# Kernel optimization log

Measured on AMD Instinct MI355X. Metric: run time of the kernel, lower is better.

The kernel has to match this reference:

```python
import jax, jax.numpy as jnp
import numpy as np

N = 50000          # total nodes in batch
E = 800000         # total edges (avg degree 16)
G = 512            # number of graphs in batch
H = 64             # hidden_channels
L = 5              # num_layers
C_IN = 1           # in_channels
NUM_CLASSES = 2
BN_EPS = 1e-5


def setup_inputs() -> dict:
    key = jax.random.key(0)
    ks = jax.random.split(key, 12)
    x = jax.random.normal(ks[0], (N, C_IN), dtype=jnp.float32)
    edge_index = jax.random.randint(ks[1], (2, E), 0, N, dtype=jnp.int64)
    batch = jnp.sort(jax.random.randint(ks[2], (N,), 0, G, dtype=jnp.int64))
    s = 0.1
    # GINConv MLP params: layer0 input is C_IN, layers 1..4 input is H
    w1_0 = jax.random.normal(ks[3], (C_IN, H), dtype=jnp.float32) * s
    w1_rest = jax.random.normal(ks[4], (L - 1, H, H), dtype=jnp.float32) * s
    b1 = jax.random.normal(ks[5], (L, H), dtype=jnp.float32) * s
    gamma_mlp = jnp.ones((L, H), dtype=jnp.float32)
    beta_mlp = jnp.zeros((L, H), dtype=jnp.float32)
    w2 = jax.random.normal(ks[6], (L, H, H), dtype=jnp.float32) * s
    b2 = jax.random.normal(ks[7], (L, H), dtype=jnp.float32) * s
    # outer per-layer BatchNorm (BasicGNN norm) params
    gamma = jnp.ones((L, H), dtype=jnp.float32)
    beta = jnp.zeros((L, H), dtype=jnp.float32)
    lin_w = jax.random.normal(ks[8], (C_IN + H * L, NUM_CLASSES), dtype=jnp.float32) * s
    lin_b = jnp.zeros((NUM_CLASSES,), dtype=jnp.float32)
    return dict(x=x, edge_index=edge_index, batch=batch, w1_0=w1_0,
                w1_rest=w1_rest, b1=b1, gamma_mlp=gamma_mlp, beta_mlp=beta_mlp,
                w2=w2, b2=b2, gamma=gamma, beta=beta, lin_w=lin_w, lin_b=lin_b)


def _bn(h, g, b):
    # training-mode batch norm over the node axis (biased variance, as torch)
    mu = h.mean(axis=0)
    var = h.var(axis=0)
    return (h - mu) * jax.lax.rsqrt(var + BN_EPS) * g + b


def _gin_backbone(x, src, dst, w1_0, w1_rest, b1, gm, bm, w2, b2, go, bo):
    h = x
    outs = []
    for l in range(L):  # fixed small layer count
        agg = jax.ops.segment_sum(h[src], dst, num_segments=N)  # sum_{j->i} h_j
        z = h + agg  # (1+eps)*h_i + agg, eps=0
        w1 = w1_0 if l == 0 else w1_rest[l - 1]
        z = z @ w1 + b1[l]
        z = jax.nn.relu(_bn(z, gm[l], bm[l]))   # MLP inner norm+act
        z = z @ w2[l] + b2[l]
        z = jax.nn.relu(_bn(z, go[l], bo[l]))   # BasicGNN norm+act (jk set)
        h = z
        outs.append(h)
    return jnp.concatenate(outs, axis=1)  # jk='cat' -> [N, H*L]


def reference(x, edge_index, batch, w1_0, w1_rest, b1, gamma_mlp, beta_mlp,
              w2, b2, gamma, beta, lin_w, lin_b):
    src, dst = edge_index[0], edge_index[1]
    node_desc = _gin_backbone(x, src, dst, w1_0, w1_rest, b1,
                              gamma_mlp, beta_mlp, w2, b2, gamma, beta)
    graph_desc = jax.ops.segment_sum(node_desc, batch, num_segments=G)  # [G, H*L]
    first_desc = jax.ops.segment_sum(x, batch, num_segments=G)          # [G, C_IN]
    gdesc = jnp.concatenate((first_desc, graph_desc), axis=1)           # [G, C_IN+H*L]
    # final dropout is identity in eval mode
    return gdesc @ lin_w + lin_b
```

## Files before the change

### kernel.cpp

```cpp
#include <hip/hip_runtime.h>

#define NN 50000
#define NE 800000
#define NG 512
#define HC 64
#define NL 5
#define GD_COLS 321
#define BN_EPS 1e-5f
#define DEG_CAP 64

#define SLICE 6250
#define ECHUNK 3125

typedef unsigned short bf16_t;
typedef unsigned int uiv4 __attribute__((ext_vector_type(4)));
typedef __attribute__((ext_vector_type(8))) short short8v;
typedef __attribute__((ext_vector_type(4))) float f32x4;
typedef __attribute__((ext_vector_type(4))) unsigned uint4v;

static __device__ __forceinline__ unsigned f2bfbits(float f) {
    unsigned u = __float_as_uint(f);
    return (u + 0x7FFFu + ((u >> 16) & 1u)) >> 16;
}
static __device__ __forceinline__ bf16_t f2bf(float f) { return (bf16_t)f2bfbits(f); }
static __device__ __forceinline__ float bf2f(bf16_t h) {
    return __uint_as_float(((unsigned)h) << 16);
}
static __device__ __forceinline__ float bflo(unsigned w) { return __uint_as_float(w << 16); }
static __device__ __forceinline__ float bfhi(unsigned w) {
    return __uint_as_float(w & 0xffff0000u);
}

static __device__ __forceinline__ void mfma_gemm_phase(
    const unsigned* zw, const unsigned* wsm, const float* __restrict__ bias,
    bf16_t* __restrict__ out, float* __restrict__ statsOut, float (*redS)[64],
    float (*redQ)[64], int r0, int t, int lane, int wid) {
    int l15 = lane & 15, l4 = lane >> 4;
    int tr = wid >> 1;
    int tc0 = (wid & 1) * 2;
    f32x4 d0 = {0.f, 0.f, 0.f, 0.f}, d1 = {0.f, 0.f, 0.f, 0.f};
    const unsigned* arow = &zw[(tr * 16 + l15) * 33];
    const unsigned* brow0 = &wsm[(tc0 * 16 + l15) * 33];
    const unsigned* brow1 = &wsm[((tc0 + 1) * 16 + l15) * 33];
#pragma unroll
    for (int kc = 0; kc < 2; ++kc) {
        int kb = kc * 16 + l4 * 4;
        uint4v aw = {arow[kb], arow[kb + 1], arow[kb + 2], arow[kb + 3]};
        uint4v bw0 = {brow0[kb], brow0[kb + 1], brow0[kb + 2], brow0[kb + 3]};
        uint4v bw1 = {brow1[kb], brow1[kb + 1], brow1[kb + 2], brow1[kb + 3]};
        short8v af = __builtin_bit_cast(short8v, aw);
        d0 = __builtin_amdgcn_mfma_f32_16x16x32_bf16(af, __builtin_bit_cast(short8v, bw0), d0,
                                                     0, 0, 0);
        d1 = __builtin_amdgcn_mfma_f32_16x16x32_bf16(af, __builtin_bit_cast(short8v, bw1), d1,
                                                     0, 0, 0);
    }
    int c0 = tc0 * 16 + l15, c1 = c0 + 16;
    float bv0 = bias[c0], bv1 = bias[c1];
    float s0 = 0.f, q0 = 0.f, s1 = 0.f, q1 = 0.f;
#pragma unroll
    for (int j = 0; j < 4; ++j) {
        int gr = r0 + tr * 16 + l4 * 4 + j;
        if (gr < NN) {
            float v0 = d0[j] + bv0, v1 = d1[j] + bv1;
            out[(size_t)gr * HC + c0] = f2bf(v0);
            out[(size_t)gr * HC + c1] = f2bf(v1);
            s0 += v0;
            q0 += v0 * v0;
            s1 += v1;
            q1 += v1 * v1;
        }
    }
    s0 += __shfl_xor(s0, 16); s0 += __shfl_xor(s0, 32);
    q0 += __shfl_xor(q0, 16); q0 += __shfl_xor(q0, 32);
    s1 += __shfl_xor(s1, 16); s1 += __shfl_xor(s1, 32);
    q1 += __shfl_xor(q1, 16); q1 += __shfl_xor(q1, 32);
    if (l4 == 0) { redS[wid][c0] = s0; redQ[wid][c0] = q0; }
    else if (l4 == 1) { redS[wid][c1] = s1; redQ[wid][c1] = q1; }
    else if (l4 == 2) { redS[wid][c0 ^ 32] = 0.f; redQ[wid][c0 ^ 32] = 0.f; }
    else { redS[wid][c1 ^ 32] = 0.f; redQ[wid][c1 ^ 32] = 0.f; }
    __syncthreads();
    if (t < 64) {
        float ts = 0.f, t2 = 0.f;
#pragma unroll
        for (int k = 0; k < 8; ++k) {
            ts += redS[k][t];
            t2 += redQ[k][t];
        }
        atomicAdd(&statsOut[t], ts);
        atomicAdd(&statsOut[64 + t], t2);
    }
}

__global__ __launch_bounds__(256) void scatter_kernel(const int* __restrict__ ei,
                                                      int* __restrict__ cnt,
                                                      unsigned short* __restrict__ ssrc,
                                                      float* __restrict__ stats,
                                                      float* __restrict__ gdesc) {
    int t = threadIdx.x;
    int g = blockIdx.x & 7;
    int c = blockIdx.x >> 3;
    int gt = blockIdx.x * 256 + t;
    int total = gridDim.x * 256;
    for (int i = gt; i < NL * 256; i += total) stats[i] = 0.f;
    for (int i = gt; i < NG * GD_COLS; i += total) gdesc[i] = 0.f;
    int lo = g * SLICE, hi = lo + SLICE;
    int e0 = c * ECHUNK;
    int e1 = e0 + ECHUNK;
    if (e1 > NE) e1 = NE;
    for (int e = e0 + t; e < e1; e += 256) {
        int d = ei[NE + e];
        if (d >= lo && d < hi) {
            int s = ei[e];
            int pos = atomicAdd(&cnt[d], 1);
            if (pos < DEG_CAP) ssrc[(d << 6) + pos] = (unsigned short)s;
        }
    }
}

__global__ __launch_bounds__(256) void layer0_kernel(
    const float* __restrict__ x, const int* __restrict__ cnt,
    const unsigned short* __restrict__ ssrc, const float* __restrict__ w,
    const float* __restrict__ bias, const int* __restrict__ batch, float* __restrict__ gdesc,
    bf16_t* __restrict__ y, float* __restrict__ stats) {
    __shared__ float z0p[256];
    __shared__ float z0s[64];
    int t = threadIdx.x, lane = t & 63, wid = t >> 6;
    int r0 = blockIdx.x * 64;
    if (t < 64) {
        int i = r0 + t;
        if (i < NN) atomicAdd(&gdesc[batch[i] * GD_COLS], x[i]);
    }
    {
        int node = t >> 2, sub = t & 3;
        int i = r0 + node;
        float acc = 0.f;
        if (i < NN) {
            int deg = cnt[i];
            if (deg > DEG_CAP) deg = DEG_CAP;
            int pa = i << 6;
            for (int p = sub; p < deg; p += 4) acc += x[ssrc[pa + p]];
            if (sub == 0) acc += x[i];
        }
        z0p[t] = acc;
    }
    __syncthreads();
    if (t < 64) z0s[t] = z0p[4 * t] + z0p[4 * t + 1] + z0p[4 * t + 2] + z0p[4 * t + 3];
    __syncthreads();
    float wv = w[lane], bv = bias[lane];
    float s = 0.f, s2 = 0.f;
    for (int j = 0; j < 16; ++j) {
        int r = r0 + wid * 16 + j;
        if (r < NN) {
            float v = z0s[wid * 16 + j] * wv + bv;
            y[r * HC + lane] = f2bf(v);
            s += v;
            s2 += v * v;
        }
    }
    __shared__ float ls[256], ls2[256];
    ls[t] = s;
    ls2[t] = s2;
    __syncthreads();
    if (wid == 0) {
        float ts = ls[lane] + ls[64 + lane] + ls[128 + lane] + ls[192 + lane];
        float t2 = ls2[lane] + ls2[64 + lane] + ls2[128 + lane] + ls2[192 + lane];
        atomicAdd(&stats[lane], ts);
        atomicAdd(&stats[64 + lane], t2);
    }
}

__global__ __launch_bounds__(512, 2) void gather_gemm_kernel(
    const bf16_t* __restrict__ u, const float* __restrict__ statsPrev,
    const float* __restrict__ gPrev, const float* __restrict__ bPrev,
    const int* __restrict__ cnt, const unsigned short* __restrict__ ssrc,
    const float* __restrict__ w, const float* __restrict__ bias, const int* __restrict__ batch,
    float* __restrict__ gdesc, int layerPrev, bf16_t* __restrict__ out,
    float* __restrict__ statsOut) {
    __shared__ unsigned zw[64 * 33];
    __shared__ unsigned wsm[64 * 33];
    __shared__ float a1[64], s1[64];
    __shared__ float redS[8][64], redQ[8][64];
    int t = threadIdx.x, lane = t & 63, wid = t >> 6;
    int r0 = blockIdx.x * 64;
    int li = lane & 7;
    int gq = lane >> 3;
    int gbase = lane & 56;
    int nB = r0 + wid * 8 + gq;
    uiv4 myidx = {0, 0, 0, 0};
    uiv4 selfv = {0, 0, 0, 0};
    int degB = 0;
    if (nB < NN) {
        degB = cnt[nB];
        if (degB > DEG_CAP) degB = DEG_CAP;
        myidx = *(const uiv4*)&ssrc[((size_t)nB << 6) + li * 8];
        selfv = *(const uiv4*)&u[(size_t)nB * HC + li * 8];
    }
    uiv4 rv0[8];
    {
        unsigned w0 = __shfl(myidx[0], gbase);
        unsigned w1 = __shfl(myidx[1], gbase);
        unsigned w2 = __shfl(myidx[2], gbase);
        unsigned w3 = __shfl(myidx[3], gbase);
        int id[8] = {(int)(w0 & 0xffff), (int)(w0 >> 16), (int)(w1 & 0xffff),
                     (int)(w1 >> 16),    (int)(w2 & 0xffff), (int)(w2 >> 16),
                     (int)(w3 & 0xffff), (int)(w3 >> 16)};
#pragma unroll
        for (int e = 0; e < 8; ++e)
            rv0[e] = *(const uiv4*)&u[(size_t)id[e] * HC + li * 8];
    }
    if (t < 64) {
        float mu = statsPrev[t] * (1.0f / NN);
        float var = statsPrev[64 + t] * (1.0f / NN) - mu * mu;
        float a = gPrev[t] * rsqrtf(var + BN_EPS);
        a1[t] = a;
        s1[t] = bPrev[t] - mu * a;
    }
    for (int idx = t; idx < 2048; idx += 512) {
        int kk = idx >> 6, c = idx & 63;
        unsigned lo = f2bfbits(w[(2 * kk) * 64 + c]);
        unsigned hi = f2bfbits(w[(2 * kk + 1) * 64 + c]);
        wsm[c * 33 + kk] = lo | (hi << 16);
    }
    __syncthreads();
    {
        float a8[8], s8[8];
#pragma unroll
        for (int c = 0; c < 8; ++c) {
            a8[c] = a1[li * 8 + c];
            s8[c] = s1[li * 8 + c];
        }
        float acc[8];
        if (nB < NN) {
            acc[0] = fmaxf(bflo(selfv[0]) * a8[0] + s8[0], 0.f);
            acc[1] = fmaxf(bfhi(selfv[0]) * a8[1] + s8[1], 0.f);
            acc[2] = fmaxf(bflo(selfv[1]) * a8[2] + s8[2], 0.f);
            acc[3] = fmaxf(bfhi(selfv[1]) * a8[3] + s8[3], 0.f);
            acc[4] = fmaxf(bflo(selfv[2]) * a8[4] + s8[4], 0.f);
            acc[5] = fmaxf(bfhi(selfv[2]) * a8[5] + s8[5], 0.f);
            acc[6] = fmaxf(bflo(selfv[3]) * a8[6] + s8[6], 0.f);
            acc[7] = fmaxf(bfhi(selfv[3]) * a8[7] + s8[7], 0.f);
        } else {
#pragma unroll
            for (int c = 0; c < 8; ++c) acc[c] = 0.f;
        }
        if (degB > 0) {
            uiv4 rv[8];
#pragma unroll
            for (int e = 0; e < 8; ++e) rv[e] = rv0[e];
            int cntA = degB < 8 ? degB : 8;
            for (int b = 1; cntA > 0; ++b) {
                uiv4 nv[8];
                int cntB = 0;
                if (b * 8 < degB) {
                    unsigned w0 = __shfl(myidx[0], gbase + b);
                    unsigned w1 = __shfl(myidx[1], gbase + b);
                    unsigned w2 = __shfl(myidx[2], gbase + b);
                    unsigned w3 = __shfl(myidx[3], gbase + b);
                    int id[8] = {(int)(w0 & 0xffff), (int)(w0 >> 16), (int)(w1 & 0xffff),
                                 (int)(w1 >> 16),    (int)(w2 & 0xffff), (int)(w2 >> 16),
                                 (int)(w3 & 0xffff), (int)(w3 >> 16)};
#pragma unroll
                    for (int e = 0; e < 8; ++e)
                        nv[e] = *(const uiv4*)&u[(size_t)id[e] * HC + li * 8];
                    cntB = degB - b * 8;
                    if (cntB > 8) cntB = 8;
                }
#pragma unroll
                for (int e = 0; e < 8; ++e) {
                    float v0 = fmaxf(bflo(rv[e][0]) * a8[0] + s8[0], 0.f);
                    float v1 = fmaxf(bfhi(rv[e][0]) * a8[1] + s8[1], 0.f);
                    float v2 = fmaxf(bflo(rv[e][1]) * a8[2] + s8[2], 0.f);
                    float v3 = fmaxf(bfhi(rv[e][1]) * a8[3] + s8[3], 0.f);
                    float v4 = fmaxf(bflo(rv[e][2]) * a8[4] + s8[4], 0.f);
                    float v5 = fmaxf(bfhi(rv[e][2]) * a8[5] + s8[5], 0.f);
                    float v6 = fmaxf(bflo(rv[e][3]) * a8[6] + s8[6], 0.f);
                    float v7 = fmaxf(bfhi(rv[e][3]) * a8[7] + s8[7], 0.f);
                    if (e < cntA) {
                        acc[0] += v0;
                        acc[1] += v1;
                        acc[2] += v2;
                        acc[3] += v3;
                        acc[4] += v4;
                        acc[5] += v5;
                        acc[6] += v6;
                        acc[7] += v7;
                    }
                }
#pragma unroll
                for (int e = 0; e < 8; ++e) rv[e] = nv[e];
                cntA = cntB;
            }
        }
        int lr = wid * 8 + gq;
        unsigned* zp = &zw[lr * 33 + li * 4];
        zp[0] = f2bfbits(acc[0]) | (f2bfbits(acc[1]) << 16);
        zp[1] = f2bfbits(acc[2]) | (f2bfbits(acc[3]) << 16);
        zp[2] = f2bfbits(acc[4]) | (f2bfbits(acc[5]) << 16);
        zp[3] = f2bfbits(acc[6]) | (f2bfbits(acc[7]) << 16);
    }
    {
        float av = a1[lane], sv = s1[lane];
        int col = 1 + layerPrev * HC + lane;
        float gacc = 0.f;
        int cur = -1;
        for (int j = 0; j < 8; ++j) {
            int gr = r0 + wid * 8 + j;
            if (gr < NN) {
                float hv = fmaxf(bf2f(u[(size_t)gr * HC + lane]) * av + sv, 0.f);
                int gid = batch[gr];
                if (gid != cur) {
                    if (cur >= 0) atomicAdd(&gdesc[cur * GD_COLS + col], gacc);
                    cur = gid;
                    gacc = 0.f;
                }
                gacc += hv;
            }
        }
        if (cur >= 0) atomicAdd(&gdesc[cur * GD_COLS + col], gacc);
    }
    __syncthreads();
    mfma_gemm_phase(zw, wsm, bias, out, statsOut, redS, redQ, r0, t, lane, wid);
}

__global__ __launch_bounds__(512) void gemm128_norm_kernel(
    const bf16_t* __restrict__ in, const float* __restrict__ w, const float* __restrict__ bias,
    const float* __restrict__ statsIn, const float* __restrict__ gIn,
    const float* __restrict__ bIn, bf16_t* __restrict__ out, float* __restrict__ statsOut) {
    __shared__ unsigned zw[128 * 33];
    __shared__ unsigned wsm[64 * 33];
    __shared__ float a1[64], s1[64];
    __shared__ float redS[8][64], redQ[8][64];
    int t = threadIdx.x, lane = t & 63, wid = t >> 6;
    int r0 = blockIdx.x * 128;
    if (t < 64) {
        float mu = statsIn[t] * (1.0f / NN);
        float var = statsIn[64 + t] * (1.0f / NN) - mu * mu;
        float a = gIn[t] * rsqrtf(var + BN_EPS);
        a1[t] = a;
        s1[t] = bIn[t] - mu * a;
    }
    for (int idx = t; idx < 2048; idx += 512) {
        int kk = idx >> 6, c = idx & 63;
        unsigned lo = f2bfbits(w[(2 * kk) * 64 + c]);
        unsigned hi = f2bfbits(w[(2 * kk + 1) * 64 + c]);
        wsm[c * 33 + kk] = lo | (hi << 16);
    }
    __syncthreads();
    for (int idx = t; idx < 1024; idx += 512) {
        int off = idx * 8;
        int r = off >> 6;
        int k = off & 63;
        uiv4 wv4 = {0u, 0u, 0u, 0u};
        int gr = r0 + r;
        if (gr < NN) wv4 = *(const uiv4*)&in[(size_t)gr * HC + k];
        unsigned* zp = &zw[r * 33 + (k >> 1)];
#pragma unroll
        for (int j = 0; j < 4; ++j) {
            unsigned word = wv4[j];
            int kk = k + 2 * j;
            float v0 = fmaxf(bflo(word) * a1[kk] + s1[kk], 0.f);
            float v1 = fmaxf(bfhi(word) * a1[kk + 1] + s1[kk + 1], 0.f);
            zp[j] = f2bfbits(v0) | (f2bfbits(v1) << 16);
        }
    }
    __syncthreads();
    int l15 = lane & 15, l4 = lane >> 4;
    const unsigned* arow = &zw[(wid * 16 + l15) * 33];
    f32x4 d[4];
#pragma unroll
    for (int tc = 0; tc < 4; ++tc) d[tc] = (f32x4){0.f, 0.f, 0.f, 0.f};
#pragma unroll
    for (int kc = 0; kc < 2; ++kc) {
        int kb = kc * 16 + l4 * 4;
        uint4v aw = {arow[kb], arow[kb + 1], arow[kb + 2], arow[kb + 3]};
        short8v af = __builtin_bit_cast(short8v, aw);
#pragma unroll
        for (int tc = 0; tc < 4; ++tc) {
            const unsigned* brow = &wsm[(tc * 16 + l15) * 33];
            uint4v bw = {brow[kb], brow[kb + 1], brow[kb + 2], brow[kb + 3]};
            d[tc] = __builtin_amdgcn_mfma_f32_16x16x32_bf16(af, __builtin_bit_cast(short8v, bw),
                                                            d[tc], 0, 0, 0);
        }
    }
    float ss[4], qq[4];
#pragma unroll
    for (int tc = 0; tc < 4; ++tc) {
        int cc = tc * 16 + l15;
        float bv = bias[cc];
        float s = 0.f, q = 0.f;
#pragma unroll
        for (int j = 0; j < 4; ++j) {
            int gr = r0 + wid * 16 + l4 * 4 + j;
            if (gr < NN) {
                float v = d[tc][j] + bv;
                out[(size_t)gr * HC + cc] = f2bf(v);
                s += v;
                q += v * v;
            }
        }
        s += __shfl_xor(s, 16); s += __shfl_xor(s, 32);
        q += __shfl_xor(q, 16); q += __shfl_xor(q, 32);
        ss[tc] = s;
        qq[tc] = q;
    }
    if (lane < 16) {
#pragma unroll
        for (int tc = 0; tc < 4; ++tc) {
            redS[wid][tc * 16 + lane] = ss[tc];
            redQ[wid][tc * 16 + lane] = qq[tc];
        }
    }
    __syncthreads();
    if (t < 64) {
        float ts = 0.f, t2 = 0.f;
#pragma unroll
        for (int k = 0; k < 8; ++k) {
            ts += redS[k][t];
            t2 += redQ[k][t];
        }
        atomicAdd(&statsOut[t], ts);
        atomicAdd(&statsOut[64 + t], t2);
    }
}

#define CHK 16
__global__ void gdesc_last_kernel(const bf16_t* __restrict__ u, const float* __restrict__ stats,
                                  const float* __restrict__ g, const float* __restrict__ b,
                                  const int* __restrict__ batch, float* __restrict__ gdesc,
                                  int layer) {
    int lane = threadIdx.x & 63;
    int wid = threadIdx.x >> 6;
    int i0 = (blockIdx.x * 4 + wid) * CHK;
    if (i0 >= NN) return;
    float mu = stats[lane] * (1.0f / NN);
    float var = stats[64 + lane] * (1.0f / NN) - mu * mu;
    float a = g[lane] * rsqrtf(var + BN_EPS);
    float s = b[lane] - mu * a;
    int col = 1 + layer * HC + lane;
    float acc = 0.f;
    int cur = -1;
    int iend = i0 + CHK;
    if (iend > NN) iend = NN;
    for (int i = i0; i < iend; ++i) {
        int gid = batch[i];
        if (gid != cur) {
            if (cur >= 0) atomicAdd(&gdesc[cur * GD_COLS + col], acc);
            cur = gid;
            acc = 0.f;
        }
        acc += fmaxf(bf2f(u[i * HC + lane]) * a + s, 0.f);
    }
    if (cur >= 0) atomicAdd(&gdesc[cur * GD_COLS + col], acc);
}

__global__ void final_gemm_kernel(const float* __restrict__ gdesc, const float* __restrict__ lw,
                                  const float* __restrict__ lb, float* __restrict__ out) {
    int g = blockIdx.x;
    int lane = threadIdx.x;
    float a0 = 0.f, a1 = 0.f;
    for (int j = lane; j < GD_COLS; j += 64) {
        float v = gdesc[g * GD_COLS + j];
        a0 += v * lw[j * 2 + 0];
        a1 += v * lw[j * 2 + 1];
    }
    for (int off = 32; off > 0; off >>= 1) {
        a0 += __shfl_down(a0, off);
        a1 += __shfl_down(a1, off);
    }
    if (lane == 0) {
        out[g * 2 + 0] = a0 + lb[0];
        out[g * 2 + 1] = a1 + lb[1];
    }
}

extern "C" void kernel_launch(void* const* d_in, const int* in_sizes, int n_in, void* d_out,
                              int out_size, void* d_ws, size_t ws_size, hipStream_t stream) {
    const float* x = (const float*)d_in[0];
    const int* ei = (const int*)d_in[1];
    const int* batch = (const int*)d_in[2];
    const float* w1_0 = (const float*)d_in[3];
    const float* w1_rest = (const float*)d_in[4];
    const float* b1 = (const float*)d_in[5];
    const float* gm = (const float*)d_in[6];
    const float* bm = (const float*)d_in[7];
    const float* w2 = (const float*)d_in[8];
    const float* b2 = (const float*)d_in[9];
    const float* go = (const float*)d_in[10];
    const float* bo = (const float*)d_in[11];
    const float* lw = (const float*)d_in[12];
    const float* lb = (const float*)d_in[13];
    float* out = (float*)d_out;

    float* stats = (float*)d_ws;
    float* gdesc = stats + NL * 256;
    bf16_t* ybuf = (bf16_t*)(gdesc + (size_t)NG * GD_COLS + 64);
    bf16_t* ubuf = ybuf + (size_t)NN * HC;
    int* cnt = (int*)(ubuf + (size_t)NN * HC);
    unsigned short* ssrc = (unsigned short*)(cnt + NN);

    hipMemsetAsync(cnt, 0, NN * sizeof(int), stream);

    scatter_kernel<<<2048, 256, 0, stream>>>(ei, cnt, ssrc, stats, gdesc);

    layer0_kernel<<<(NN + 63) / 64, 256, 0, stream>>>(x, cnt, ssrc, w1_0, b1, batch, gdesc, ybuf,
                                                      stats);
    gemm128_norm_kernel<<<(NN + 127) / 128, 512, 0, stream>>>(ybuf, w2, b2, stats, gm, bm, ubuf,
                                                              stats + 128);
    for (int l = 1; l < NL; ++l) {
        float* st1 = stats + l * 256;
        float* st2 = st1 + 128;
        float* stPrev = stats + (l - 1) * 256 + 128;
        gather_gemm_kernel<<<(NN + 63) / 64, 512, 0, stream>>>(
            ubuf, stPrev, go + (l - 1) * HC, bo + (l - 1) * HC, cnt, ssrc,
            w1_rest + (size_t)(l - 1) * HC * HC, b1 + l * HC, batch, gdesc, l - 1, ybuf, st1);
        gemm128_norm_kernel<<<(NN + 127) / 128, 512, 0, stream>>>(
            ybuf, w2 + (size_t)l * HC * HC, b2 + l * HC, st1, gm + l * HC, bm + l * HC, ubuf, st2);
    }
    gdesc_last_kernel<<<(NN + 4 * CHK - 1) / (4 * CHK), 256, 0, stream>>>(
        ubuf, stats + 4 * 256 + 128, go + 4 * HC, bo + 4 * HC, batch, gdesc, 4);
    final_gemm_kernel<<<NG, 64, 0, stream>>>(gdesc, lw, lb, out);
}
```

Baseline: 402.2 us.

## Sort nodes by in-degree to balance gather work across wavefronts

Builds a degree histogram in layer 0, then a prefix sum and a fill kernel that produce a permutation of nodes grouped by capped in-degree. The gather+GEMM kernels process nodes in this permuted order and scatter their outputs back to the original row positions. The goal is to make the nodes sharing a wavefront have similar neighbour counts, reducing divergence and idle lanes in the neighbour gather. The cost is two extra launches, heavily contended atomics on a few histogram and offset counters, and scattered rather than contiguous output row writes.

```diff
diff --git a/kernel.cpp b/kernel.cpp
--- a/kernel.cpp
+++ b/kernel.cpp
@@ -33,8 +33,8 @@
 
 static __device__ __forceinline__ void mfma_gemm_phase(
     const unsigned* zw, const unsigned* wsm, const float* __restrict__ bias,
-    bf16_t* __restrict__ out, float* __restrict__ statsOut, float (*redS)[64],
-    float (*redQ)[64], int r0, int t, int lane, int wid) {
+    const int* __restrict__ perm, bf16_t* __restrict__ out, float* __restrict__ statsOut,
+    float (*redS)[64], float (*redQ)[64], int r0, int t, int lane, int wid) {
     int l15 = lane & 15, l4 = lane >> 4;
     int tr = wid >> 1;
     int tc0 = (wid & 1) * 2;
@@ -59,8 +59,9 @@
     float s0 = 0.f, q0 = 0.f, s1 = 0.f, q1 = 0.f;
 #pragma unroll
     for (int j = 0; j < 4; ++j) {
-        int gr = r0 + tr * 16 + l4 * 4 + j;
-        if (gr < NN) {
+        int rr = r0 + tr * 16 + l4 * 4 + j;
+        if (rr < NN) {
+            int gr = perm ? perm[rr] : rr;
             float v0 = d0[j] + bv0, v1 = d1[j] + bv1;
             out[(size_t)gr * HC + c0] = f2bf(v0);
             out[(size_t)gr * HC + c1] = f2bf(v1);
@@ -121,7 +122,7 @@
     const float* __restrict__ x, const int* __restrict__ cnt,
     const unsigned short* __restrict__ ssrc, const float* __restrict__ w,
     const float* __restrict__ bias, const int* __restrict__ batch, float* __restrict__ gdesc,
-    bf16_t* __restrict__ y, float* __restrict__ stats) {
+    bf16_t* __restrict__ y, float* __restrict__ stats, int* __restrict__ hist) {
     __shared__ float z0p[256];
     __shared__ float z0s[64];
     int t = threadIdx.x, lane = t & 63, wid = t >> 6;
@@ -137,6 +138,7 @@
         if (i < NN) {
             int deg = cnt[i];
             if (deg > DEG_CAP) deg = DEG_CAP;
+            if (sub == 0) atomicAdd(&hist[deg], 1);
             int pa = i << 6;
             for (int p = sub; p < deg; p += 4) acc += x[ssrc[pa + p]];
             if (sub == 0) acc += x[i];
@@ -169,13 +171,35 @@
     }
 }
 
+__global__ void perm_prefix_kernel(const int* __restrict__ hist, int* __restrict__ offs) {
+    if (threadIdx.x == 0) {
+        int run = 0;
+        for (int d = 0; d <= DEG_CAP; ++d) {
+            offs[d] = run;
+            run += hist[d];
+        }
+    }
+}
+
+__global__ __launch_bounds__(256) void perm_fill_kernel(const int* __restrict__ cnt,
+                                                        int* __restrict__ offs,
+                                                        int* __restrict__ perm) {
+    int i = blockIdx.x * 256 + threadIdx.x;
+    if (i < NN) {
+        int d = cnt[i];
+        if (d > DEG_CAP) d = DEG_CAP;
+        int pos = atomicAdd(&offs[d], 1);
+        perm[pos] = i;
+    }
+}
+
 __global__ __launch_bounds__(512, 2) void gather_gemm_kernel(
     const bf16_t* __restrict__ u, const float* __restrict__ statsPrev,
     const float* __restrict__ gPrev, const float* __restrict__ bPrev,
     const int* __restrict__ cnt, const unsigned short* __restrict__ ssrc,
-    const float* __restrict__ w, const float* __restrict__ bias, const int* __restrict__ batch,
-    float* __restrict__ gdesc, int layerPrev, bf16_t* __restrict__ out,
-    float* __restrict__ statsOut) {
+    const int* __restrict__ perm, const float* __restrict__ w, const float* __restrict__ bias,
+    const int* __restrict__ batch, float* __restrict__ gdesc, int layerPrev,
+    bf16_t* __restrict__ out, float* __restrict__ statsOut) {
     __shared__ unsigned zw[64 * 33];
     __shared__ unsigned wsm[64 * 33];
     __shared__ float a1[64], s1[64];
@@ -185,7 +209,8 @@
     int li = lane & 7;
     int gq = lane >> 3;
     int gbase = lane & 56;
-    int nB = r0 + wid * 8 + gq;
+    int rIdx = r0 + wid * 8 + gq;
+    int nB = rIdx < NN ? perm[rIdx] : NN;
     uiv4 myidx = {0, 0, 0, 0};
     uiv4 selfv = {0, 0, 0, 0};
     int degB = 0;
@@ -319,7 +344,7 @@
         if (cur >= 0) atomicAdd(&gdesc[cur * GD_COLS + col], gacc);
     }
     __syncthreads();
-    mfma_gemm_phase(zw, wsm, bias, out, statsOut, redS, redQ, r0, t, lane, wid);
+    mfma_gemm_phase(zw, wsm, bias, perm, out, statsOut, redS, redQ, r0, t, lane, wid);
 }
 
 __global__ __launch_bounds__(512) void gemm128_norm_kernel(
@@ -496,14 +521,19 @@
     bf16_t* ybuf = (bf16_t*)(gdesc + (size_t)NG * GD_COLS + 64);
     bf16_t* ubuf = ybuf + (size_t)NN * HC;
     int* cnt = (int*)(ubuf + (size_t)NN * HC);
-    unsigned short* ssrc = (unsigned short*)(cnt + NN);
-
-    hipMemsetAsync(cnt, 0, NN * sizeof(int), stream);
+    int* hist = cnt + NN;
+    int* offs = hist + 80;
+    int* perm = offs + 80;
+    unsigned short* ssrc = (unsigned short*)(perm + NN);
+
+    hipMemsetAsync(cnt, 0, (NN + 160) * sizeof(int), stream);
 
     scatter_kernel<<<2048, 256, 0, stream>>>(ei, cnt, ssrc, stats, gdesc);
 
     layer0_kernel<<<(NN + 63) / 64, 256, 0, stream>>>(x, cnt, ssrc, w1_0, b1, batch, gdesc, ybuf,
-                                                      stats);
+                                                      stats, hist);
+    perm_prefix_kernel<<<1, 64, 0, stream>>>(hist, offs);
+    perm_fill_kernel<<<(NN + 255) / 256, 256, 0, stream>>>(cnt, offs, perm);
     gemm128_norm_kernel<<<(NN + 127) / 128, 512, 0, stream>>>(ybuf, w2, b2, stats, gm, bm, ubuf,
                                                               stats + 128);
     for (int l = 1; l < NL; ++l) {
@@ -511,7 +541,7 @@
         float* st2 = st1 + 128;
         float* stPrev = stats + (l - 1) * 256 + 128;
         gather_gemm_kernel<<<(NN + 63) / 64, 512, 0, stream>>>(
-            ubuf, stPrev, go + (l - 1) * HC, bo + (l - 1) * HC, cnt, ssrc,
+            ubuf, stPrev, go + (l - 1) * HC, bo + (l - 1) * HC, cnt, ssrc, perm,
             w1_rest + (size_t)(l - 1) * HC * HC, b1 + l * HC, batch, gdesc, l - 1, ybuf, st1);
         gemm128_norm_kernel<<<(NN + 127) / 128, 512, 0, stream>>>(
             ybuf, w2 + (size_t)l * HC * HC, b2 + l * HC, st1, gm + l * HC, bm + l * HC, ubuf, st2);
```

New measurement: 635.4 us. 58.0% more time.

## Materialize normalized activations before gather instead of normalizing per-edge

Applied to the files above, without the earlier changes.

Splits the outer BatchNorm+ReLU out of the gather kernel into a separate pass that writes normalized bf16 activations to a new buffer and also accumulates graph descriptors. The gather kernel then sums pre-activated neighbor rows, so it no longer recomputes the affine+ReLU for every edge and carries no gdesc atomics. In exchange it adds a kernel launch per layer and an extra full read/write of the N x 64 activation tensor. The gather also drops a __syncthreads, since it no longer needs the a1/s1 shared values.

```diff
diff --git a/kernel.cpp b/kernel.cpp
--- a/kernel.cpp
+++ b/kernel.cpp
@@ -169,265 +169,11 @@
     }
 }
 
-__global__ __launch_bounds__(512, 2) void gather_gemm_kernel(
-    const bf16_t* __restrict__ u, const float* __restrict__ statsPrev,
-    const float* __restrict__ gPrev, const float* __restrict__ bPrev,
-    const int* __restrict__ cnt, const unsigned short* __restrict__ ssrc,
-    const float* __restrict__ w, const float* __restrict__ bias, const int* __restrict__ batch,
-    float* __restrict__ gdesc, int layerPrev, bf16_t* __restrict__ out,
-    float* __restrict__ statsOut) {
-    __shared__ unsigned zw[64 * 33];
-    __shared__ unsigned wsm[64 * 33];
-    __shared__ float a1[64], s1[64];
-    __shared__ float redS[8][64], redQ[8][64];
-    int t = threadIdx.x, lane = t & 63, wid = t >> 6;
-    int r0 = blockIdx.x * 64;
-    int li = lane & 7;
-    int gq = lane >> 3;
-    int gbase = lane & 56;
-    int nB = r0 + wid * 8 + gq;
-    uiv4 myidx = {0, 0, 0, 0};
-    uiv4 selfv = {0, 0, 0, 0};
-    int degB = 0;
-    if (nB < NN) {
-        degB = cnt[nB];
-        if (degB > DEG_CAP) degB = DEG_CAP;
-        myidx = *(const uiv4*)&ssrc[((size_t)nB << 6) + li * 8];
-        selfv = *(const uiv4*)&u[(size_t)nB * HC + li * 8];
-    }
-    uiv4 rv0[8];
-    {
-        unsigned w0 = __shfl(myidx[0], gbase);
-        unsigned w1 = __shfl(myidx[1], gbase);
-        unsigned w2 = __shfl(myidx[2], gbase);
-        unsigned w3 = __shfl(myidx[3], gbase);
-        int id[8] = {(int)(w0 & 0xffff), (int)(w0 >> 16), (int)(w1 & 0xffff),
-                     (int)(w1 >> 16),    (int)(w2 & 0xffff), (int)(w2 >> 16),
-                     (int)(w3 & 0xffff), (int)(w3 >> 16)};
-#pragma unroll
-        for (int e = 0; e < 8; ++e)
-            rv0[e] = *(const uiv4*)&u[(size_t)id[e] * HC + li * 8];
-    }
-    if (t < 64) {
-        float mu = statsPrev[t] * (1.0f / NN);
-        float var = statsPrev[64 + t] * (1.0f / NN) - mu * mu;
-        float a = gPrev[t] * rsqrtf(var + BN_EPS);
-        a1[t] = a;
-        s1[t] = bPrev[t] - mu * a;
-    }
-    for (int idx = t; idx < 2048; idx += 512) {
-        int kk = idx >> 6, c = idx & 63;
-        unsigned lo = f2bfbits(w[(2 * kk) * 64 + c]);
-        unsigned hi = f2bfbits(w[(2 * kk + 1) * 64 + c]);
-        wsm[c * 33 + kk] = lo | (hi << 16);
-    }
-    __syncthreads();
-    {
-        float a8[8], s8[8];
-#pragma unroll
-        for (int c = 0; c < 8; ++c) {
-            a8[c] = a1[li * 8 + c];
-            s8[c] = s1[li * 8 + c];
-        }
-        float acc[8];
-        if (nB < NN) {
-            acc[0] = fmaxf(bflo(selfv[0]) * a8[0] + s8[0], 0.f);
-            acc[1] = fmaxf(bfhi(selfv[0]) * a8[1] + s8[1], 0.f);
-            acc[2] = fmaxf(bflo(selfv[1]) * a8[2] + s8[2], 0.f);
-            acc[3] = fmaxf(bfhi(selfv[1]) * a8[3] + s8[3], 0.f);
-            acc[4] = fmaxf(bflo(selfv[2]) * a8[4] + s8[4], 0.f);
-            acc[5] = fmaxf(bfhi(selfv[2]) * a8[5] + s8[5], 0.f);
-            acc[6] = fmaxf(bflo(selfv[3]) * a8[6] + s8[6], 0.f);
-            acc[7] = fmaxf(bfhi(selfv[3]) * a8[7] + s8[7], 0.f);
-        } else {
-#pragma unroll
-            for (int c = 0; c < 8; ++c) acc[c] = 0.f;
-        }
-        if (degB > 0) {
-            uiv4 rv[8];
-#pragma unroll
-            for (int e = 0; e < 8; ++e) rv[e] = rv0[e];
-            int cntA = degB < 8 ? degB : 8;
-            for (int b = 1; cntA > 0; ++b) {
-                uiv4 nv[8];
-                int cntB = 0;
-                if (b * 8 < degB) {
-                    unsigned w0 = __shfl(myidx[0], gbase + b);
-                    unsigned w1 = __shfl(myidx[1], gbase + b);
-                    unsigned w2 = __shfl(myidx[2], gbase + b);
-                    unsigned w3 = __shfl(myidx[3], gbase + b);
-                    int id[8] = {(int)(w0 & 0xffff), (int)(w0 >> 16), (int)(w1 & 0xffff),
-                                 (int)(w1 >> 16),    (int)(w2 & 0xffff), (int)(w2 >> 16),
-                                 (int)(w3 & 0xffff), (int)(w3 >> 16)};
-#pragma unroll
-                    for (int e = 0; e < 8; ++e)
-                        nv[e] = *(const uiv4*)&u[(size_t)id[e] * HC + li * 8];
-                    cntB = degB - b * 8;
-                    if (cntB > 8) cntB = 8;
-                }
-#pragma unroll
-                for (int e = 0; e < 8; ++e) {
-                    float v0 = fmaxf(bflo(rv[e][0]) * a8[0] + s8[0], 0.f);
-                    float v1 = fmaxf(bfhi(rv[e][0]) * a8[1] + s8[1], 0.f);
-                    float v2 = fmaxf(bflo(rv[e][1]) * a8[2] + s8[2], 0.f);
-                    float v3 = fmaxf(bfhi(rv[e][1]) * a8[3] + s8[3], 0.f);
-                    float v4 = fmaxf(bflo(rv[e][2]) * a8[4] + s8[4], 0.f);
-                    float v5 = fmaxf(bfhi(rv[e][2]) * a8[5] + s8[5], 0.f);
-                    float v6 = fmaxf(bflo(rv[e][3]) * a8[6] + s8[6], 0.f);
-                    float v7 = fmaxf(bfhi(rv[e][3]) * a8[7] + s8[7], 0.f);
-                    if (e < cntA) {
-                        acc[0] += v0;
-                        acc[1] += v1;
-                        acc[2] += v2;
-                        acc[3] += v3;
-                        acc[4] += v4;
-                        acc[5] += v5;
-                        acc[6] += v6;
-                        acc[7] += v7;
-                    }
-                }
-#pragma unroll
-                for (int e = 0; e < 8; ++e) rv[e] = nv[e];
-                cntA = cntB;
-            }
-        }
-        int lr = wid * 8 + gq;
-        unsigned* zp = &zw[lr * 33 + li * 4];
-        zp[0] = f2bfbits(acc[0]) | (f2bfbits(acc[1]) << 16);
-        zp[1] = f2bfbits(acc[2]) | (f2bfbits(acc[3]) << 16);
-        zp[2] = f2bfbits(acc[4]) | (f2bfbits(acc[5]) << 16);
-        zp[3] = f2bfbits(acc[6]) | (f2bfbits(acc[7]) << 16);
-    }
-    {
-        float av = a1[lane], sv = s1[lane];
-        int col = 1 + layerPrev * HC + lane;
-        float gacc = 0.f;
-        int cur = -1;
-        for (int j = 0; j < 8; ++j) {
-            int gr = r0 + wid * 8 + j;
-            if (gr < NN) {
-                float hv = fmaxf(bf2f(u[(size_t)gr * HC + lane]) * av + sv, 0.f);
-                int gid = batch[gr];
-                if (gid != cur) {
-                    if (cur >= 0) atomicAdd(&gdesc[cur * GD_COLS + col], gacc);
-                    cur = gid;
-                    gacc = 0.f;
-                }
-                gacc += hv;
-            }
-        }
-        if (cur >= 0) atomicAdd(&gdesc[cur * GD_COLS + col], gacc);
-    }
-    __syncthreads();
-    mfma_gemm_phase(zw, wsm, bias, out, statsOut, redS, redQ, r0, t, lane, wid);
-}
-
-__global__ __launch_bounds__(512) void gemm128_norm_kernel(
-    const bf16_t* __restrict__ in, const float* __restrict__ w, const float* __restrict__ bias,
-    const float* __restrict__ statsIn, const float* __restrict__ gIn,
-    const float* __restrict__ bIn, bf16_t* __restrict__ out, float* __restrict__ statsOut) {
-    __shared__ unsigned zw[128 * 33];
-    __shared__ unsigned wsm[64 * 33];
-    __shared__ float a1[64], s1[64];
-    __shared__ float redS[8][64], redQ[8][64];
-    int t = threadIdx.x, lane = t & 63, wid = t >> 6;
-    int r0 = blockIdx.x * 128;
-    if (t < 64) {
-        float mu = statsIn[t] * (1.0f / NN);
-        float var = statsIn[64 + t] * (1.0f / NN) - mu * mu;
-        float a = gIn[t] * rsqrtf(var + BN_EPS);
-        a1[t] = a;
-        s1[t] = bIn[t] - mu * a;
-    }
-    for (int idx = t; idx < 2048; idx += 512) {
-        int kk = idx >> 6, c = idx & 63;
-        unsigned lo = f2bfbits(w[(2 * kk) * 64 + c]);
-        unsigned hi = f2bfbits(w[(2 * kk + 1) * 64 + c]);
-        wsm[c * 33 + kk] = lo | (hi << 16);
-    }
-    __syncthreads();
-    for (int idx = t; idx < 1024; idx += 512) {
-        int off = idx * 8;
-        int r = off >> 6;
-        int k = off & 63;
-        uiv4 wv4 = {0u, 0u, 0u, 0u};
-        int gr = r0 + r;
-        if (gr < NN) wv4 = *(const uiv4*)&in[(size_t)gr * HC + k];
-        unsigned* zp = &zw[r * 33 + (k >> 1)];
-#pragma unroll
-        for (int j = 0; j < 4; ++j) {
-            unsigned word = wv4[j];
-            int kk = k + 2 * j;
-            float v0 = fmaxf(bflo(word) * a1[kk] + s1[kk], 0.f);
-            float v1 = fmaxf(bfhi(word) * a1[kk + 1] + s1[kk + 1], 0.f);
-            zp[j] = f2bfbits(v0) | (f2bfbits(v1) << 16);
-        }
-    }
-    __syncthreads();
-    int l15 = lane & 15, l4 = lane >> 4;
-    const unsigned* arow = &zw[(wid * 16 + l15) * 33];
-    f32x4 d[4];
-#pragma unroll
-    for (int tc = 0; tc < 4; ++tc) d[tc] = (f32x4){0.f, 0.f, 0.f, 0.f};
-#pragma unroll
-    for (int kc = 0; kc < 2; ++kc) {
-        int kb = kc * 16 + l4 * 4;
-        uint4v aw = {arow[kb], arow[kb + 1], arow[kb + 2], arow[kb + 3]};
-        short8v af = __builtin_bit_cast(short8v, aw);
-#pragma unroll
-        for (int tc = 0; tc < 4; ++tc) {
-            const unsigned* brow = &wsm[(tc * 16 + l15) * 33];
-            uint4v bw = {brow[kb], brow[kb + 1], brow[kb + 2], brow[kb + 3]};
-            d[tc] = __builtin_amdgcn_mfma_f32_16x16x32_bf16(af, __builtin_bit_cast(short8v, bw),
-                                                            d[tc], 0, 0, 0);
-        }
-    }
-    float ss[4], qq[4];
-#pragma unroll
-    for (int tc = 0; tc < 4; ++tc) {
-        int cc = tc * 16 + l15;
-        float bv = bias[cc];
-        float s = 0.f, q = 0.f;
-#pragma unroll
-        for (int j = 0; j < 4; ++j) {
-            int gr = r0 + wid * 16 + l4 * 4 + j;
-            if (gr < NN) {
-                float v = d[tc][j] + bv;
-                out[(size_t)gr * HC + cc] = f2bf(v);
-                s += v;
-                q += v * v;
-            }
-        }
-        s += __shfl_xor(s, 16); s += __shfl_xor(s, 32);
-        q += __shfl_xor(q, 16); q += __shfl_xor(q, 32);
-        ss[tc] = s;
-        qq[tc] = q;
-    }
-    if (lane < 16) {
-#pragma unroll
-        for (int tc = 0; tc < 4; ++tc) {
-            redS[wid][tc * 16 + lane] = ss[tc];
-            redQ[wid][tc * 16 + lane] = qq[tc];
-        }
-    }
-    __syncthreads();
-    if (t < 64) {
-        float ts = 0.f, t2 = 0.f;
-#pragma unroll
-        for (int k = 0; k < 8; ++k) {
-            ts += redS[k][t];
-            t2 += redQ[k][t];
-        }
-        atomicAdd(&statsOut[t], ts);
-        atomicAdd(&statsOut[64 + t], t2);
-    }
-}
-
 #define CHK 16
-__global__ void gdesc_last_kernel(const bf16_t* __restrict__ u, const float* __restrict__ stats,
-                                  const float* __restrict__ g, const float* __restrict__ b,
-                                  const int* __restrict__ batch, float* __restrict__ gdesc,
-                                  int layer) {
+__global__ void act_gdesc_kernel(const bf16_t* __restrict__ u, const float* __restrict__ stats,
+                                 const float* __restrict__ g, const float* __restrict__ b,
+                                 const int* __restrict__ batch, float* __restrict__ gdesc,
+                                 int layer, bf16_t* __restrict__ hout) {
     int lane = threadIdx.x & 63;
     int wid = threadIdx.x >> 6;
     int i0 = (blockIdx.x * 4 + wid) * CHK;
@@ -448,9 +194,227 @@
             cur = gid;
             acc = 0.f;
         }
-        acc += fmaxf(bf2f(u[i * HC + lane]) * a + s, 0.f);
+        float hv = fmaxf(bf2f(u[(size_t)i * HC + lane]) * a + s, 0.f);
+        if (hout) hout[(size_t)i * HC + lane] = f2bf(hv);
+        acc += hv;
     }
     if (cur >= 0) atomicAdd(&gdesc[cur * GD_COLS + col], acc);
+}
+
+__global__ __launch_bounds__(512, 2) void gather_gemm_kernel(
+    const bf16_t* __restrict__ h, const int* __restrict__ cnt,
+    const unsigned short* __restrict__ ssrc, const float* __restrict__ w,
+    const float* __restrict__ bias, bf16_t* __restrict__ out, float* __restrict__ statsOut) {
+    __shared__ unsigned zw[64 * 33];
+    __shared__ unsigned wsm[64 * 33];
+    __shared__ float redS[8][64], redQ[8][64];
+    int t = threadIdx.x, lane = t & 63, wid = t >> 6;
+    int r0 = blockIdx.x * 64;
+    int li = lane & 7;
+    int gq = lane >> 3;
+    int gbase = lane & 56;
+    int nB = r0 + wid * 8 + gq;
+    uiv4 myidx = {0, 0, 0, 0};
+    uiv4 selfv = {0, 0, 0, 0};
+    int degB = 0;
+    if (nB < NN) {
+        degB = cnt[nB];
+        if (degB > DEG_CAP) degB = DEG_CAP;
+        myidx = *(const uiv4*)&ssrc[((size_t)nB << 6) + li * 8];
+        selfv = *(const uiv4*)&h[(size_t)nB * HC + li * 8];
+    }
+    uiv4 rv0[8];
+    {
+        unsigned w0 = __shfl(myidx[0], gbase);
+        unsigned w1 = __shfl(myidx[1], gbase);
+        unsigned w2 = __shfl(myidx[2], gbase);
+        unsigned w3 = __shfl(myidx[3], gbase);
+        int id[8] = {(int)(w0 & 0xffff), (int)(w0 >> 16), (int)(w1 & 0xffff),
+                     (int)(w1 >> 16),    (int)(w2 & 0xffff), (int)(w2 >> 16),
+                     (int)(w3 & 0xffff), (int)(w3 >> 16)};
+#pragma unroll
+        for (int e = 0; e < 8; ++e)
+            rv0[e] = *(const uiv4*)&h[(size_t)id[e] * HC + li * 8];
+    }
+    for (int idx = t; idx < 2048; idx += 512) {
+        int kk = idx >> 6, c = idx & 63;
+        unsigned lo = f2bfbits(w[(2 * kk) * 64 + c]);
+        unsigned hi = f2bfbits(w[(2 * kk + 1) * 64 + c]);
+        wsm[c * 33 + kk] = lo | (hi << 16);
+    }
+    {
+        float acc[8];
+        if (nB < NN) {
+            acc[0] = bflo(selfv[0]);
+            acc[1] = bfhi(selfv[0]);
+            acc[2] = bflo(selfv[1]);
+            acc[3] = bfhi(selfv[1]);
+            acc[4] = bflo(selfv[2]);
+            acc[5] = bfhi(selfv[2]);
+            acc[6] = bflo(selfv[3]);
+            acc[7] = bfhi(selfv[3]);
+        } else {
+#pragma unroll
+            for (int c = 0; c < 8; ++c) acc[c] = 0.f;
+        }
+        if (degB > 0) {
+            uiv4 rv[8];
+#pragma unroll
+            for (int e = 0; e < 8; ++e) rv[e] = rv0[e];
+            int cntA = degB < 8 ? degB : 8;
+            for (int b = 1; cntA > 0; ++b) {
+                uiv4 nv[8];
+                int cntB = 0;
+                if (b * 8 < degB) {
+                    unsigned w0 = __shfl(myidx[0], gbase + b);
+                    unsigned w1 = __shfl(myidx[1], gbase + b);
+                    unsigned w2 = __shfl(myidx[2], gbase + b);
+                    unsigned w3 = __shfl(myidx[3], gbase + b);
+                    int id[8] = {(int)(w0 & 0xffff), (int)(w0 >> 16), (int)(w1 & 0xffff),
+                                 (int)(w1 >> 16),    (int)(w2 & 0xffff), (int)(w2 >> 16),
+                                 (int)(w3 & 0xffff), (int)(w3 >> 16)};
+#pragma unroll
+                    for (int e = 0; e < 8; ++e)
+                        nv[e] = *(const uiv4*)&h[(size_t)id[e] * HC + li * 8];
+                    cntB = degB - b * 8;
+                    if (cntB > 8) cntB = 8;
+                }
+#pragma unroll
+                for (int e = 0; e < 8; ++e) {
+                    float v0 = bflo(rv[e][0]);
+                    float v1 = bfhi(rv[e][0]);
+                    float v2 = bflo(rv[e][1]);
+                    float v3 = bfhi(rv[e][1]);
+                    float v4 = bflo(rv[e][2]);
+                    float v5 = bfhi(rv[e][2]);
+                    float v6 = bflo(rv[e][3]);
+                    float v7 = bfhi(rv[e][3]);
+                    if (e < cntA) {
+                        acc[0] += v0;
+                        acc[1] += v1;
+                        acc[2] += v2;
+                        acc[3] += v3;
+                        acc[4] += v4;
+                        acc[5] += v5;
+                        acc[6] += v6;
+                        acc[7] += v7;
+                    }
+                }
+#pragma unroll
+                for (int e = 0; e < 8; ++e) rv[e] = nv[e];
+                cntA = cntB;
+            }
+        }
+        int lr = wid * 8 + gq;
+        unsigned* zp = &zw[lr * 33 + li * 4];
+        zp[0] = f2bfbits(acc[0]) | (f2bfbits(acc[1]) << 16);
+        zp[1] = f2bfbits(acc[2]) | (f2bfbits(acc[3]) << 16);
+        zp[2] = f2bfbits(acc[4]) | (f2bfbits(acc[5]) << 16);
+        zp[3] = f2bfbits(acc[6]) | (f2bfbits(acc[7]) << 16);
+    }
+    __syncthreads();
+    mfma_gemm_phase(zw, wsm, bias, out, statsOut, redS, redQ, r0, t, lane, wid);
+}
+
+__global__ __launch_bounds__(512) void gemm128_norm_kernel(
+    const bf16_t* __restrict__ in, const float* __restrict__ w, const float* __restrict__ bias,
+    const float* __restrict__ statsIn, const float* __restrict__ gIn,
+    const float* __restrict__ bIn, bf16_t* __restrict__ out, float* __restrict__ statsOut) {
+    __shared__ unsigned zw[128 * 33];
+    __shared__ unsigned wsm[64 * 33];
+    __shared__ float a1[64], s1[64];
+    __shared__ float redS[8][64], redQ[8][64];
+    int t = threadIdx.x, lane = t & 63, wid = t >> 6;
+    int r0 = blockIdx.x * 128;
+    if (t < 64) {
+        float mu = statsIn[t] * (1.0f / NN);
+        float var = statsIn[64 + t] * (1.0f / NN) - mu * mu;
+        float a = gIn[t] * rsqrtf(var + BN_EPS);
+        a1[t] = a;
+        s1[t] = bIn[t] - mu * a;
+    }
+    for (int idx = t; idx < 2048; idx += 512) {
+        int kk = idx >> 6, c = idx & 63;
+        unsigned lo = f2bfbits(w[(2 * kk) * 64 + c]);
+        unsigned hi = f2bfbits(w[(2 * kk + 1) * 64 + c]);
+        wsm[c * 33 + kk] = lo | (hi << 16);
+    }
+    __syncthreads();
+    for (int idx = t; idx < 1024; idx += 512) {
+        int off = idx * 8;
+        int r = off >> 6;
+        int k = off & 63;
+        uiv4 wv4 = {0u, 0u, 0u, 0u};
+        int gr = r0 + r;
+        if (gr < NN) wv4 = *(const uiv4*)&in[(size_t)gr * HC + k];
+        unsigned* zp = &zw[r * 33 + (k >> 1)];
+#pragma unroll
+        for (int j = 0; j < 4; ++j) {
+            unsigned word = wv4[j];
+            int kk = k + 2 * j;
+            float v0 = fmaxf(bflo(word) * a1[kk] + s1[kk], 0.f);
+            float v1 = fmaxf(bfhi(word) * a1[kk + 1] + s1[kk + 1], 0.f);
+            zp[j] = f2bfbits(v0) | (f2bfbits(v1) << 16);
+        }
+    }
+    __syncthreads();
+    int l15 = lane & 15, l4 = lane >> 4;
+    const unsigned* arow = &zw[(wid * 16 + l15) * 33];
+    f32x4 d[4];
+#pragma unroll
+    for (int tc = 0; tc < 4; ++tc) d[tc] = (f32x4){0.f, 0.f, 0.f, 0.f};
+#pragma unroll
+    for (int kc = 0; kc < 2; ++kc) {
+        int kb = kc * 16 + l4 * 4;
+        uint4v aw = {arow[kb], arow[kb + 1], arow[kb + 2], arow[kb + 3]};
+        short8v af = __builtin_bit_cast(short8v, aw);
+#pragma unroll
+        for (int tc = 0; tc < 4; ++tc) {
+            const unsigned* brow = &wsm[(tc * 16 + l15) * 33];
+            uint4v bw = {brow[kb], brow[kb + 1], brow[kb + 2], brow[kb + 3]};
+            d[tc] = __builtin_amdgcn_mfma_f32_16x16x32_bf16(af, __builtin_bit_cast(short8v, bw),
+                                                            d[tc], 0, 0, 0);
+        }
+    }
+    float ss[4], qq[4];
+#pragma unroll
+    for (int tc = 0; tc < 4; ++tc) {
+        int cc = tc * 16 + l15;
+        float bv = bias[cc];
+        float s = 0.f, q = 0.f;
+#pragma unroll
+        for (int j = 0; j < 4; ++j) {
+            int gr = r0 + wid * 16 + l4 * 4 + j;
+            if (gr < NN) {
+                float v = d[tc][j] + bv;
+                out[(size_t)gr * HC + cc] = f2bf(v);
+                s += v;
+                q += v * v;
+            }
+        }
+        s += __shfl_xor(s, 16); s += __shfl_xor(s, 32);
+        q += __shfl_xor(q, 16); q += __shfl_xor(q, 32);
+        ss[tc] = s;
+        qq[tc] = q;
+    }
+    if (lane < 16) {
+#pragma unroll
+        for (int tc = 0; tc < 4; ++tc) {
+            redS[wid][tc * 16 + lane] = ss[tc];
+            redQ[wid][tc * 16 + lane] = qq[tc];
+        }
+    }
+    __syncthreads();
+    if (t < 64) {
+        float ts = 0.f, t2 = 0.f;
+#pragma unroll
+        for (int k = 0; k < 8; ++k) {
+            ts += redS[k][t];
+            t2 += redQ[k][t];
+        }
+        atomicAdd(&statsOut[t], ts);
+        atomicAdd(&statsOut[64 + t], t2);
+    }
 }
 
 __global__ void final_gemm_kernel(const float* __restrict__ gdesc, const float* __restrict__ lw,
@@ -497,6 +461,7 @@
     bf16_t* ubuf = ybuf + (size_t)NN * HC;
     int* cnt = (int*)(ubuf + (size_t)NN * HC);
     unsigned short* ssrc = (unsigned short*)(cnt + NN);
+    bf16_t* hbuf = (bf16_t*)(ssrc + (size_t)NN * 64);
 
     hipMemsetAsync(cnt, 0, NN * sizeof(int), stream);
 
@@ -510,13 +475,14 @@
         float* st1 = stats + l * 256;
         float* st2 = st1 + 128;
         float* stPrev = stats + (l - 1) * 256 + 128;
+        act_gdesc_kernel<<<(NN + 4 * CHK - 1) / (4 * CHK), 256, 0, stream>>>(
+            ubuf, stPrev, go + (l - 1) * HC, bo + (l - 1) * HC, batch, gdesc, l - 1, hbuf);
         gather_gemm_kernel<<<(NN + 63) / 64, 512, 0, stream>>>(
-            ubuf, stPrev, go + (l - 1) * HC, bo + (l - 1) * HC, cnt, ssrc,
-            w1_rest + (size_t)(l - 1) * HC * HC, b1 + l * HC, batch, gdesc, l - 1, ybuf, st1);
+            hbuf, cnt, ssrc, w1_rest + (size_t)(l - 1) * HC * HC, b1 + l * HC, ybuf, st1);
         gemm128_norm_kernel<<<(NN + 127) / 128, 512, 0, stream>>>(
             ybuf, w2 + (size_t)l * HC * HC, b2 + l * HC, st1, gm + l * HC, bm + l * HC, ubuf, st2);
     }
-    gdesc_last_kernel<<<(NN + 4 * CHK - 1) / (4 * CHK), 256, 0, stream>>>(
-        ubuf, stats + 4 * 256 + 128, go + 4 * HC, bo + 4 * HC, batch, gdesc, 4);
+    act_gdesc_kernel<<<(NN + 4 * CHK - 1) / (4 * CHK), 256, 0, stream>>>(
+        ubuf, stats + 4 * 256 + 128, go + 4 * HC, bo + 4 * HC, batch, gdesc, 4, nullptr);
     final_gemm_kernel<<<NG, 64, 0, stream>>>(gdesc, lw, lb, out);
 }
```

After: 450.7 us. 1.12x slower.
